# Kernel optimization log

Hardware: AMD Instinct MI355X
Metric: run time of the kernel (lower is better)

Reference implementation:

```python
import jax, jax.numpy as jnp
import numpy as np

N, B, S, F_DIM, E = 100000, 4096, 32, 256, 256


def _linear_params(key, fan_in, fan_out):
    kw, kb = jax.random.split(key)
    bound = 1.0 / np.sqrt(fan_in)
    W = jax.random.uniform(kw, (fan_in, fan_out), jnp.float32, -bound, bound)
    b = jax.random.uniform(kb, (fan_out,), jnp.float32, -bound, bound)
    return W, b


def setup_inputs() -> dict:
    key = jax.random.key(0)
    ks = jax.random.split(key, 10)
    Wm, bm = _linear_params(ks[4], F_DIM, E)
    Wq, bq = _linear_params(ks[5], F_DIM, E)
    Wk, bk = _linear_params(ks[6], F_DIM, E)
    Wv, bv = _linear_params(ks[7], F_DIM, E)
    Wc, bc = _linear_params(ks[8], 2 * E, E)
    return {
        "nodes": jax.random.randint(ks[0], (B,), 0, N),
        "neigh_mean": jax.random.randint(ks[1], (B, S), 0, N),
        "neigh_attn": jax.random.randint(ks[2], (B, S), 0, N),
        "id2feat": jax.random.normal(ks[3], (N, F_DIM), jnp.float32),
        "Wm": Wm, "bm": bm,
        "Wq": Wq, "bq": bq,
        "Wk": Wk, "bk": bk,
        "Wv": Wv, "bv": bv,
        "Wc": Wc, "bc": bc,
    }


def reference(nodes, neigh_mean, neigh_attn, id2feat,
              Wm, bm, Wq, bq, Wk, bk, Wv, bv, Wc, bc):
    self_feats = id2feat[nodes]                                   # [B, F]

    # MeanAggregator1: per-row mean of W(id2feat[neighbors]).
    # (mean(W x + b) == W mean(x) + b by linearity; all rows have S neighbors)
    ctx = jnp.mean(id2feat[neigh_mean], axis=1) @ Wm + bm          # [B, E]

    # AttnAggregator1: self-query attention over [neighbors ; self].
    neigh = id2feat[neigh_attn]                                    # [B, S, F]
    cat = jnp.concatenate([neigh, self_feats[:, None, :]], axis=1)  # [B, S+1, F]
    Q = self_feats @ Wq + bq                                       # [B, E]
    K = cat @ Wk + bk                                              # [B, S+1, E]
    V = cat @ Wv + bv                                              # [B, S+1, E]
    scores = jnp.einsum('be,bse->bs', Q, K)                        # [B, S+1]
    # Torch mask loop with uniform neighbor length S masks column S (the self slot)
    pad_mask = jnp.arange(S + 1) >= S                              # [S+1]
    scores = jnp.where(pad_mask[None, :], -jnp.inf, scores)
    attn = jax.nn.softmax(scores, axis=-1)
    mix = jnp.einsum('bs,bse->be', attn, V)                        # [B, E]

    combined = jnp.tanh(jnp.concatenate([mix, ctx], axis=-1) @ Wc + bc)  # [B, E]
    norm = jnp.linalg.norm(combined, axis=-1, keepdims=True)
    return combined / jnp.maximum(norm, 1e-12)                     # F.normalize(p=2)
```

## Files before the change

### kernel.cpp

```cpp
#include <hip/hip_runtime.h>
#include <hip/hip_fp16.h>
#include <math.h>

#define S_NEI 32

__global__ __launch_bounds__(256) void transpose256(const float* __restrict__ in,
                                                    float* __restrict__ outT) {
    __shared__ float tile[32][33];
    const int bx = blockIdx.x * 32, by = blockIdx.y * 32;
    const int x = threadIdx.x, y = threadIdx.y;
#pragma unroll
    for (int i = 0; i < 32; i += 8)
        tile[y + i][x] = in[(by + y + i) * 256 + bx + x];
    __syncthreads();
#pragma unroll
    for (int i = 0; i < 32; i += 8)
        outT[(bx + y + i) * 256 + by + x] = tile[x][y + i];
}

template <int KT>
__device__ __forceinline__ void gemm_tile8(const float* __restrict__ A, int row0,
                                           const float* __restrict__ B,
                                           float acc[2][4], float* __restrict__ sA,
                                           float* __restrict__ sB) {
    const int t = threadIdx.x;
    const int tr = t >> 6, tc = t & 63;
    const int r = t >> 5;
    const int k1 = t & 31;
    const size_t arow = (size_t)(row0 + r) * KT;
    for (int kb = 0; kb < KT; kb += 32) {
        sA[k1 * 12 + r] = A[arow + kb + k1];
#pragma unroll
        for (int i = 0; i < 8; ++i) {
            *reinterpret_cast<float4*>(&sB[(i * 4 + tr) * 256 + tc * 4]) =
                *reinterpret_cast<const float4*>(&B[(size_t)(kb + i * 4 + tr) * 256 + tc * 4]);
        }
        __syncthreads();
#pragma unroll
        for (int k = 0; k < 32; ++k) {
            const float2 a2 = *reinterpret_cast<const float2*>(&sA[k * 12 + tr * 2]);
            const float4 b4 = *reinterpret_cast<const float4*>(&sB[k * 256 + tc * 4]);
            acc[0][0] += a2.x * b4.x; acc[0][1] += a2.x * b4.y;
            acc[0][2] += a2.x * b4.z; acc[0][3] += a2.x * b4.w;
            acc[1][0] += a2.y * b4.x; acc[1][1] += a2.y * b4.y;
            acc[1][2] += a2.y * b4.z; acc[1][3] += a2.y * b4.w;
        }
        __syncthreads();
    }
}

__global__ __launch_bounds__(256) void precompute3(const float* __restrict__ Wq,
                                                   const float* __restrict__ Wv,
                                                   const float* __restrict__ Wm,
                                                   const float* __restrict__ Wc,
                                                   const float* __restrict__ WkT,
                                                   __half* __restrict__ Wqk,
                                                   __half* __restrict__ Wfused) {
    __shared__ float sA[32 * 12];
    __shared__ float sB[32 * 256];
    float acc[2][4] = {};
    const float *Ap, *Bp;
    __half* Cp;
    switch (blockIdx.y) {
        case 0: Ap = Wq; Bp = WkT; Cp = Wqk; break;
        case 1: Ap = Wv; Bp = Wc; Cp = Wfused; break;
        default: Ap = Wm; Bp = Wc + 256 * 256; Cp = Wfused + 256 * 256; break;
    }
    const int row0 = blockIdx.x * 8;
    gemm_tile8<256>(Ap, row0, Bp, acc, sA, sB);
    const int tr = threadIdx.x >> 6, tc = threadIdx.x & 63;
#pragma unroll
    for (int i = 0; i < 2; ++i) {
        const __half2 h0 = __floats2half2_rn(acc[i][0], acc[i][1]);
        const __half2 h1 = __floats2half2_rn(acc[i][2], acc[i][3]);
        __half2* dst = reinterpret_cast<__half2*>(&Cp[(size_t)(row0 + tr * 2 + i) * 256 + tc * 4]);
        dst[0] = h0;
        dst[1] = h1;
    }
}

__global__ __launch_bounds__(256) void bias_k(const float* __restrict__ bq,
                                              const float* __restrict__ bv,
                                              const float* __restrict__ bm,
                                              const float* __restrict__ bc,
                                              const float* __restrict__ Wc,
                                              const float* __restrict__ WkT,
                                              float* __restrict__ bqk,
                                              float* __restrict__ bfull) {
    const int c = blockIdx.x;
    const int e = threadIdx.x;
    const int w = e >> 6, l = e & 63;
    float a = bq[e] * WkT[e * 256 + c];
    float v = bv[e] * Wc[e * 256 + c] + bm[e] * Wc[(256 + e) * 256 + c];
    __shared__ float redA[4], redV[4];
#pragma unroll
    for (int off = 32; off; off >>= 1) { a += __shfl_xor(a, off); v += __shfl_xor(v, off); }
    if (l == 0) { redA[w] = a; redV[w] = v; }
    __syncthreads();
    if (e == 0) {
        bqk[c] = redA[0] + redA[1] + redA[2] + redA[3];
        bfull[c] = bc[c] + redV[0] + redV[1] + redV[2] + redV[3];
    }
}


#define SAF4(k) ((k) * 4 + ((((k) >> 3)) << 2))

#define FMA44(a4, b4)                                                       \
    do {                                                                    \
        acc[0][0] += (a4).x * (b4).x; acc[0][1] += (a4).x * (b4).y;         \
        acc[0][2] += (a4).x * (b4).z; acc[0][3] += (a4).x * (b4).w;         \
        acc[1][0] += (a4).y * (b4).x; acc[1][1] += (a4).y * (b4).y;         \
        acc[1][2] += (a4).y * (b4).z; acc[1][3] += (a4).y * (b4).w;         \
        acc[2][0] += (a4).z * (b4).x; acc[2][1] += (a4).z * (b4).y;         \
        acc[2][2] += (a4).z * (b4).z; acc[2][3] += (a4).z * (b4).w;         \
        acc[3][0] += (a4).w * (b4).x; acc[3][1] += (a4).w * (b4).y;         \
        acc[3][2] += (a4).w * (b4).z; acc[3][3] += (a4).w * (b4).w;         \
    } while (0)

__device__ __forceinline__ float4 h4_to_f4(float2 raw) {
    const __half2* h = reinterpret_cast<const __half2*>(&raw);
    const float2 f0 = __half22float2(h[0]);
    const float2 f1 = __half22float2(h[1]);
    return make_float4(f0.x, f0.y, f1.x, f1.y);
}

__global__ __launch_bounds__(256, 2) void fused4(const float* __restrict__ id2feat,
                                                 const int* __restrict__ nodes,
                                                 const int* __restrict__ neigh_mean,
                                                 const int* __restrict__ neigh_attn,
                                                 const __half* __restrict__ Wqk,
                                                 const float* __restrict__ bqk,
                                                 const __half* __restrict__ Wfused,
                                                 const float* __restrict__ bfull,
                                                 float* __restrict__ out) {
    __shared__ __align__(16) char smem[18112];
    float* R0  = (float*)smem;
    float* sQk = (float*)(smem + 12480);
    int*   sIA = (int*)(smem + 16640);
    int*   sIM = (int*)(smem + 17152);

    const int t = threadIdx.x;
    const int w = t >> 6, l = t & 63;
    const int kq = w;
    const int col4 = l * 4;
    const int row0 = blockIdx.x * 4;

    if (t < 128) sIA[t] = neigh_attn[(size_t)row0 * S_NEI + t];
    else sIM[t - 128] = neigh_mean[(size_t)row0 * S_NEI + (t - 128)];

    {
        const float4 v = *reinterpret_cast<const float4*>(
            &id2feat[(size_t)nodes[row0 + w] * 256 + col4]);
        R0[SAF4(col4 + 0) + w] = v.x;
        R0[SAF4(col4 + 1) + w] = v.y;
        R0[SAF4(col4 + 2) + w] = v.z;
        R0[SAF4(col4 + 3) + w] = v.w;
    }
    __syncthreads();

    float acc[4][4] = {};

    {
        const __half* Bp = Wqk + (size_t)(kq * 64) * 256 + col4;
        float2 bufA[8], bufB[8];
#pragma unroll
        for (int j = 0; j < 8; ++j)
            bufA[j] = *reinterpret_cast<const float2*>(&Bp[(size_t)j * 256]);
        for (int kb = 0; kb < 64; kb += 16) {
#pragma unroll
            for (int j = 0; j < 8; ++j)
                bufB[j] = *reinterpret_cast<const float2*>(&Bp[(size_t)(kb + 8 + j) * 256]);
#pragma unroll
            for (int j = 0; j < 8; ++j) {
                const float4 a4 = *reinterpret_cast<const float4*>(&R0[SAF4(kq * 64 + kb + j)]);
                const float4 b4 = h4_to_f4(bufA[j]);
                FMA44(a4, b4);
            }
            if (kb + 16 < 64) {
#pragma unroll
                for (int j = 0; j < 8; ++j)
                    bufA[j] = *reinterpret_cast<const float2*>(&Bp[(size_t)(kb + 16 + j) * 256]);
            }
#pragma unroll
            for (int j = 0; j < 8; ++j) {
                const float4 a4 =
                    *reinterpret_cast<const float4*>(&R0[SAF4(kq * 64 + kb + 8 + j)]);
                const float4 b4 = h4_to_f4(bufB[j]);
                FMA44(a4, b4);
            }
        }
    }
    __syncthreads();
    if (kq) {
        float* p = R0 + ((kq - 1) * 4) * 260 + col4;
#pragma unroll
        for (int r = 0; r < 4; ++r) {
            p[r * 260 + 0] = acc[r][0]; p[r * 260 + 1] = acc[r][1];
            p[r * 260 + 2] = acc[r][2]; p[r * 260 + 3] = acc[r][3];
        }
    }
    __syncthreads();
    if (kq == 0) {
        const float4 bq4 = *reinterpret_cast<const float4*>(&bqk[col4]);
#pragma unroll
        for (int r = 0; r < 4; ++r) {
            float v0 = acc[r][0] + bq4.x, v1 = acc[r][1] + bq4.y;
            float v2 = acc[r][2] + bq4.z, v3 = acc[r][3] + bq4.w;
#pragma unroll
            for (int s = 0; s < 3; ++s) {
                const float* p = R0 + (s * 4 + r) * 260 + col4;
                v0 += p[0]; v1 += p[1]; v2 += p[2]; v3 += p[3];
            }
            sQk[r * 260 + col4 + 0] = v0; sQk[r * 260 + col4 + 1] = v1;
            sQk[r * 260 + col4 + 2] = v2; sQk[r * 260 + col4 + 3] = v3;
        }
    }
    __syncthreads();

    {
        const int b = w;
        const float4 q = *reinterpret_cast<const float4*>(&sQk[b * 260 + col4]);
        const float4* f4 = reinterpret_cast<const float4*>(id2feat);
        const int* ia = sIA + b * 32;
        const int* im = sIM + b * 32;
        float4 macc = make_float4(0.f, 0.f, 0.f, 0.f);
        float4 wa = make_float4(0.f, 0.f, 0.f, 0.f);
        float m = -1e30f, e = 0.f;
#pragma unroll
        for (int cch = 0; cch < 4; ++cch) {
            float4 r[8];
#pragma unroll
            for (int j = 0; j < 8; ++j) r[j] = f4[(size_t)ia[cch * 8 + j] * 64 + l];
#pragma unroll
            for (int j = 0; j < 8; ++j) {
                const float4 v = f4[(size_t)im[cch * 8 + j] * 64 + l];
                macc.x += v.x; macc.y += v.y; macc.z += v.z; macc.w += v.w;
            }
            float p[8];
#pragma unroll
            for (int j = 0; j < 8; ++j) {
                float s = q.x * r[j].x + q.y * r[j].y + q.z * r[j].z + q.w * r[j].w;
#pragma unroll
                for (int off = 32; off; off >>= 1) s += __shfl_xor(s, off);
                p[j] = s;
            }
            float cm = p[0];
#pragma unroll
            for (int j = 1; j < 8; ++j) cm = fmaxf(cm, p[j]);
            const float newm = fmaxf(m, cm);
            const float sc = __expf(m - newm);
            e *= sc; wa.x *= sc; wa.y *= sc; wa.z *= sc; wa.w *= sc;
#pragma unroll
            for (int j = 0; j < 8; ++j) {
                const float g = __expf(p[j] - newm);
                e += g;
                wa.x += g * r[j].x; wa.y += g * r[j].y;
                wa.z += g * r[j].z; wa.w += g * r[j].w;
            }
            m = newm;
        }
        const float inv = 1.0f / e;
        const float mixv[4] = {wa.x * inv, wa.y * inv, wa.z * inv, wa.w * inv};
        const float mev[4] = {macc.x * (1.f / 32), macc.y * (1.f / 32),
                              macc.z * (1.f / 32), macc.w * (1.f / 32)};
#pragma unroll
        for (int c = 0; c < 4; ++c) {
            R0[SAF4(col4 + c) + b] = mixv[c];
            R0[SAF4(256 + col4 + c) + b] = mev[c];
        }
    }
    __syncthreads();

#pragma unroll
    for (int r = 0; r < 4; ++r)
#pragma unroll
        for (int c = 0; c < 4; ++c) acc[r][c] = 0.f;
    {
        const __half* Bp = Wfused + (size_t)(kq * 128) * 256 + col4;
        float2 bufA[8], bufB[8];
#pragma unroll
        for (int j = 0; j < 8; ++j)
            bufA[j] = *reinterpret_cast<const float2*>(&Bp[(size_t)j * 256]);
        for (int kb = 0; kb < 128; kb += 16) {
#pragma unroll
            for (int j = 0; j < 8; ++j)
                bufB[j] = *reinterpret_cast<const float2*>(&Bp[(size_t)(kb + 8 + j) * 256]);
#pragma unroll
            for (int j = 0; j < 8; ++j) {
                const float4 a4 =
                    *reinterpret_cast<const float4*>(&R0[SAF4(kq * 128 + kb + j)]);
                const float4 b4 = h4_to_f4(bufA[j]);
                FMA44(a4, b4);
            }
            if (kb + 16 < 128) {
#pragma unroll
                for (int j = 0; j < 8; ++j)
                    bufA[j] = *reinterpret_cast<const float2*>(&Bp[(size_t)(kb + 16 + j) * 256]);
            }
#pragma unroll
            for (int j = 0; j < 8; ++j) {
                const float4 a4 =
                    *reinterpret_cast<const float4*>(&R0[SAF4(kq * 128 + kb + 8 + j)]);
                const float4 b4 = h4_to_f4(bufB[j]);
                FMA44(a4, b4);
            }
        }
    }
    __syncthreads();
    if (kq) {
        float* p = R0 + ((kq - 1) * 4) * 260 + col4;
#pragma unroll
        for (int r = 0; r < 4; ++r) {
            p[r * 260 + 0] = acc[r][0]; p[r * 260 + 1] = acc[r][1];
            p[r * 260 + 2] = acc[r][2]; p[r * 260 + 3] = acc[r][3];
        }
    }
    __syncthreads();
    if (kq == 0) {
        const float4 bf4 = *reinterpret_cast<const float4*>(&bfull[col4]);
#pragma unroll
        for (int r = 0; r < 4; ++r) {
            float v0 = acc[r][0] + bf4.x, v1 = acc[r][1] + bf4.y;
            float v2 = acc[r][2] + bf4.z, v3 = acc[r][3] + bf4.w;
#pragma unroll
            for (int s = 0; s < 3; ++s) {
                const float* p = R0 + (s * 4 + r) * 260 + col4;
                v0 += p[0]; v1 += p[1]; v2 += p[2]; v3 += p[3];
            }
            v0 = tanhf(v0); v1 = tanhf(v1); v2 = tanhf(v2); v3 = tanhf(v3);
            float sq = v0 * v0 + v1 * v1 + v2 * v2 + v3 * v3;
#pragma unroll
            for (int off = 32; off; off >>= 1) sq += __shfl_xor(sq, off);
            const float invn = 1.0f / fmaxf(sqrtf(sq), 1e-12f);
            *reinterpret_cast<float4*>(&out[(size_t)(row0 + r) * 256 + col4]) =
                make_float4(v0 * invn, v1 * invn, v2 * invn, v3 * invn);
        }
    }
}

extern "C" void kernel_launch(void* const* d_in, const int* in_sizes, int n_in,
                              void* d_out, int out_size, void* d_ws, size_t ws_size,
                              hipStream_t stream) {
    const int* nodes      = (const int*)d_in[0];
    const int* neigh_mean = (const int*)d_in[1];
    const int* neigh_attn = (const int*)d_in[2];
    const float* id2feat  = (const float*)d_in[3];
    const float* Wm = (const float*)d_in[4];
    const float* bm = (const float*)d_in[5];
    const float* Wq = (const float*)d_in[6];
    const float* bq = (const float*)d_in[7];
    const float* Wk = (const float*)d_in[8];
    const float* Wv = (const float*)d_in[10];
    const float* bv = (const float*)d_in[11];
    const float* Wc = (const float*)d_in[12];
    const float* bc = (const float*)d_in[13];
    float* out = (float*)d_out;

    const int B = in_sizes[0];

    float* ws      = (float*)d_ws;
    float* WkT     = ws;
    __half* Wqk_h  = (__half*)(ws + 65536);
    __half* Wfus_h = (__half*)(ws + 98304);
    float* bqk     = ws + 163840;
    float* bfull   = ws + 164096;

    transpose256<<<dim3(8, 8), dim3(32, 8), 0, stream>>>(Wk, WkT);
    precompute3<<<dim3(32, 3), 256, 0, stream>>>(Wq, Wv, Wm, Wc, WkT, Wqk_h, Wfus_h);
    bias_k<<<256, 256, 0, stream>>>(bq, bv, bm, bc, Wc, WkT, bqk, bfull);
    fused4<<<B / 4, 256, 0, stream>>>(id2feat, nodes, neigh_mean, neigh_attn,
                                      Wqk_h, bqk, Wfus_h, bfull, out);
}
```

Measured before the change: 78.20 us.

## Process two rows per block and split neighbor gather across wave pairs

The fused kernel now handles 2 batch rows per block instead of 4, doubling the grid to B/2 blocks. Each row's 32-neighbor gather and online softmax is split across two waves (16 neighbors each), and the partial max, sum, weighted-V and mean results are merged through shared memory with a rescale. This raises parallelism and memory-level concurrency for the gather phase. In exchange, each block reads the fp16 weight matrices for only half as many rows, which doubles total weight traffic, and an extra sync and merge step is added.

```diff
diff --git a/kernel.cpp b/kernel.cpp
--- a/kernel.cpp
+++ b/kernel.cpp
@@ -104,18 +104,14 @@
 }
 
 
-#define SAF4(k) ((k) * 4 + ((((k) >> 3)) << 2))
-
-#define FMA44(a4, b4)                                                       \
+#define SAF2(k) ((k) * 2 + (((k) >> 3) << 1))
+
+#define FMA24(a2, b4)                                                       \
     do {                                                                    \
-        acc[0][0] += (a4).x * (b4).x; acc[0][1] += (a4).x * (b4).y;         \
-        acc[0][2] += (a4).x * (b4).z; acc[0][3] += (a4).x * (b4).w;         \
-        acc[1][0] += (a4).y * (b4).x; acc[1][1] += (a4).y * (b4).y;         \
-        acc[1][2] += (a4).y * (b4).z; acc[1][3] += (a4).y * (b4).w;         \
-        acc[2][0] += (a4).z * (b4).x; acc[2][1] += (a4).z * (b4).y;         \
-        acc[2][2] += (a4).z * (b4).z; acc[2][3] += (a4).z * (b4).w;         \
-        acc[3][0] += (a4).w * (b4).x; acc[3][1] += (a4).w * (b4).y;         \
-        acc[3][2] += (a4).w * (b4).z; acc[3][3] += (a4).w * (b4).w;         \
+        acc[0][0] += (a2).x * (b4).x; acc[0][1] += (a2).x * (b4).y;         \
+        acc[0][2] += (a2).x * (b4).z; acc[0][3] += (a2).x * (b4).w;         \
+        acc[1][0] += (a2).y * (b4).x; acc[1][1] += (a2).y * (b4).y;         \
+        acc[1][2] += (a2).y * (b4).z; acc[1][3] += (a2).y * (b4).w;         \
     } while (0)
 
 __device__ __forceinline__ float4 h4_to_f4(float2 raw) {
@@ -125,7 +121,7 @@
     return make_float4(f0.x, f0.y, f1.x, f1.y);
 }
 
-__global__ __launch_bounds__(256, 2) void fused4(const float* __restrict__ id2feat,
+__global__ __launch_bounds__(256, 2) void fused2(const float* __restrict__ id2feat,
                                                  const int* __restrict__ nodes,
                                                  const int* __restrict__ neigh_mean,
                                                  const int* __restrict__ neigh_attn,
@@ -134,32 +130,33 @@
                                                  const __half* __restrict__ Wfused,
                                                  const float* __restrict__ bfull,
                                                  float* __restrict__ out) {
-    __shared__ __align__(16) char smem[18112];
-    float* R0  = (float*)smem;
-    float* sQk = (float*)(smem + 12480);
-    int*   sIA = (int*)(smem + 16640);
-    int*   sIM = (int*)(smem + 17152);
+    __shared__ __align__(16) char smem[15456];
+    float* RA  = (float*)smem;
+    float* RB  = (float*)(smem + 4608);
+    float* sQk = (float*)(smem + 12864);
+    int*   sIA = (int*)(smem + 14944);
+    int*   sIM = (int*)(smem + 15200);
 
     const int t = threadIdx.x;
     const int w = t >> 6, l = t & 63;
     const int kq = w;
     const int col4 = l * 4;
-    const int row0 = blockIdx.x * 4;
-
-    if (t < 128) sIA[t] = neigh_attn[(size_t)row0 * S_NEI + t];
-    else sIM[t - 128] = neigh_mean[(size_t)row0 * S_NEI + (t - 128)];
-
-    {
+    const int row0 = blockIdx.x * 2;
+
+    if (t < 64) sIA[t] = neigh_attn[(size_t)row0 * S_NEI + t];
+    else if (t < 128) sIM[t - 64] = neigh_mean[(size_t)row0 * S_NEI + (t - 64)];
+
+    if (w < 2) {
         const float4 v = *reinterpret_cast<const float4*>(
             &id2feat[(size_t)nodes[row0 + w] * 256 + col4]);
-        R0[SAF4(col4 + 0) + w] = v.x;
-        R0[SAF4(col4 + 1) + w] = v.y;
-        R0[SAF4(col4 + 2) + w] = v.z;
-        R0[SAF4(col4 + 3) + w] = v.w;
-    }
-    __syncthreads();
-
-    float acc[4][4] = {};
+        RA[SAF2(col4 + 0) + w] = v.x;
+        RA[SAF2(col4 + 1) + w] = v.y;
+        RA[SAF2(col4 + 2) + w] = v.z;
+        RA[SAF2(col4 + 3) + w] = v.w;
+    }
+    __syncthreads();
+
+    float acc[2][4] = {};
 
     {
         const __half* Bp = Wqk + (size_t)(kq * 64) * 256 + col4;
@@ -173,9 +170,9 @@
                 bufB[j] = *reinterpret_cast<const float2*>(&Bp[(size_t)(kb + 8 + j) * 256]);
 #pragma unroll
             for (int j = 0; j < 8; ++j) {
-                const float4 a4 = *reinterpret_cast<const float4*>(&R0[SAF4(kq * 64 + kb + j)]);
+                const float2 a2 = *reinterpret_cast<const float2*>(&RA[SAF2(kq * 64 + kb + j)]);
                 const float4 b4 = h4_to_f4(bufA[j]);
-                FMA44(a4, b4);
+                FMA24(a2, b4);
             }
             if (kb + 16 < 64) {
 #pragma unroll
@@ -184,18 +181,18 @@
             }
 #pragma unroll
             for (int j = 0; j < 8; ++j) {
-                const float4 a4 =
-                    *reinterpret_cast<const float4*>(&R0[SAF4(kq * 64 + kb + 8 + j)]);
+                const float2 a2 =
+                    *reinterpret_cast<const float2*>(&RA[SAF2(kq * 64 + kb + 8 + j)]);
                 const float4 b4 = h4_to_f4(bufB[j]);
-                FMA44(a4, b4);
+                FMA24(a2, b4);
             }
         }
     }
     __syncthreads();
     if (kq) {
-        float* p = R0 + ((kq - 1) * 4) * 260 + col4;
-#pragma unroll
-        for (int r = 0; r < 4; ++r) {
+        float* p = RB + ((kq - 1) * 2) * 260 + col4;
+#pragma unroll
+        for (int r = 0; r < 2; ++r) {
             p[r * 260 + 0] = acc[r][0]; p[r * 260 + 1] = acc[r][1];
             p[r * 260 + 2] = acc[r][2]; p[r * 260 + 3] = acc[r][3];
         }
@@ -204,12 +201,12 @@
     if (kq == 0) {
         const float4 bq4 = *reinterpret_cast<const float4*>(&bqk[col4]);
 #pragma unroll
-        for (int r = 0; r < 4; ++r) {
+        for (int r = 0; r < 2; ++r) {
             float v0 = acc[r][0] + bq4.x, v1 = acc[r][1] + bq4.y;
             float v2 = acc[r][2] + bq4.z, v3 = acc[r][3] + bq4.w;
 #pragma unroll
             for (int s = 0; s < 3; ++s) {
-                const float* p = R0 + (s * 4 + r) * 260 + col4;
+                const float* p = RB + (s * 2 + r) * 260 + col4;
                 v0 += p[0]; v1 += p[1]; v2 += p[2]; v3 += p[3];
             }
             sQk[r * 260 + col4 + 0] = v0; sQk[r * 260 + col4 + 1] = v1;
@@ -218,17 +215,17 @@
     }
     __syncthreads();
 
+    float4 wa = make_float4(0.f, 0.f, 0.f, 0.f);
+    float4 macc = make_float4(0.f, 0.f, 0.f, 0.f);
+    float m = -1e30f, e = 0.f;
     {
-        const int b = w;
+        const int b = w >> 1, h = w & 1;
         const float4 q = *reinterpret_cast<const float4*>(&sQk[b * 260 + col4]);
         const float4* f4 = reinterpret_cast<const float4*>(id2feat);
-        const int* ia = sIA + b * 32;
-        const int* im = sIM + b * 32;
-        float4 macc = make_float4(0.f, 0.f, 0.f, 0.f);
-        float4 wa = make_float4(0.f, 0.f, 0.f, 0.f);
-        float m = -1e30f, e = 0.f;
-#pragma unroll
-        for (int cch = 0; cch < 4; ++cch) {
+        const int* ia = sIA + b * 32 + h * 16;
+        const int* im = sIM + b * 32 + h * 16;
+#pragma unroll
+        for (int cch = 0; cch < 2; ++cch) {
             float4 r[8];
 #pragma unroll
             for (int j = 0; j < 8; ++j) r[j] = f4[(size_t)ia[cch * 8 + j] * 64 + l];
@@ -260,20 +257,42 @@
             }
             m = newm;
         }
-        const float inv = 1.0f / e;
-        const float mixv[4] = {wa.x * inv, wa.y * inv, wa.z * inv, wa.w * inv};
-        const float mev[4] = {macc.x * (1.f / 32), macc.y * (1.f / 32),
-                              macc.z * (1.f / 32), macc.w * (1.f / 32)};
+    }
+    {
+        float4* sW = (float4*)RB;
+        float4* sM = (float4*)(RB + 1024);
+        float* sME = RB + 2048;
+        sW[w * 64 + l] = wa;
+        sM[w * 64 + l] = macc;
+        if (l == 0) { sME[w * 2] = m; sME[w * 2 + 1] = e; }
+    }
+    __syncthreads();
+    if ((w & 1) == 0) {
+        const int b = w >> 1;
+        const float4* sW = (const float4*)RB;
+        const float4* sM = (const float4*)(RB + 1024);
+        const float* sME = RB + 2048;
+        const float m0 = sME[w * 2], e0 = sME[w * 2 + 1];
+        const float m1 = sME[(w + 1) * 2], e1 = sME[(w + 1) * 2 + 1];
+        const float M = fmaxf(m0, m1);
+        const float f0 = __expf(m0 - M), f1 = __expf(m1 - M);
+        const float inv = 1.0f / (e0 * f0 + e1 * f1);
+        const float4 w0 = sW[w * 64 + l], w1 = sW[(w + 1) * 64 + l];
+        const float4 c0 = sM[w * 64 + l], c1 = sM[(w + 1) * 64 + l];
+        const float mixv[4] = {(w0.x * f0 + w1.x * f1) * inv, (w0.y * f0 + w1.y * f1) * inv,
+                               (w0.z * f0 + w1.z * f1) * inv, (w0.w * f0 + w1.w * f1) * inv};
+        const float mev[4] = {(c0.x + c1.x) * (1.f / 32), (c0.y + c1.y) * (1.f / 32),
+                              (c0.z + c1.z) * (1.f / 32), (c0.w + c1.w) * (1.f / 32)};
 #pragma unroll
         for (int c = 0; c < 4; ++c) {
-            R0[SAF4(col4 + c) + b] = mixv[c];
-            R0[SAF4(256 + col4 + c) + b] = mev[c];
-        }
-    }
-    __syncthreads();
-
-#pragma unroll
-    for (int r = 0; r < 4; ++r)
+            RA[SAF2(col4 + c) + b] = mixv[c];
+            RA[SAF2(256 + col4 + c) + b] = mev[c];
+        }
+    }
+    __syncthreads();
+
+#pragma unroll
+    for (int r = 0; r < 2; ++r)
 #pragma unroll
         for (int c = 0; c < 4; ++c) acc[r][c] = 0.f;
     {
@@ -288,10 +307,10 @@
                 bufB[j] = *reinterpret_cast<const float2*>(&Bp[(size_t)(kb + 8 + j) * 256]);
 #pragma unroll
             for (int j = 0; j < 8; ++j) {
-                const float4 a4 =
-                    *reinterpret_cast<const float4*>(&R0[SAF4(kq * 128 + kb + j)]);
+                const float2 a2 =
+                    *reinterpret_cast<const float2*>(&RA[SAF2(kq * 128 + kb + j)]);
                 const float4 b4 = h4_to_f4(bufA[j]);
-                FMA44(a4, b4);
+                FMA24(a2, b4);
             }
             if (kb + 16 < 128) {
 #pragma unroll
@@ -300,18 +319,18 @@
             }
 #pragma unroll
             for (int j = 0; j < 8; ++j) {
-                const float4 a4 =
-                    *reinterpret_cast<const float4*>(&R0[SAF4(kq * 128 + kb + 8 + j)]);
+                const float2 a2 =
+                    *reinterpret_cast<const float2*>(&RA[SAF2(kq * 128 + kb + 8 + j)]);
                 const float4 b4 = h4_to_f4(bufB[j]);
-                FMA44(a4, b4);
+                FMA24(a2, b4);
             }
         }
     }
     __syncthreads();
     if (kq) {
-        float* p = R0 + ((kq - 1) * 4) * 260 + col4;
-#pragma unroll
-        for (int r = 0; r < 4; ++r) {
+        float* p = RB + ((kq - 1) * 2) * 260 + col4;
+#pragma unroll
+        for (int r = 0; r < 2; ++r) {
             p[r * 260 + 0] = acc[r][0]; p[r * 260 + 1] = acc[r][1];
             p[r * 260 + 2] = acc[r][2]; p[r * 260 + 3] = acc[r][3];
         }
@@ -320,12 +339,12 @@
     if (kq == 0) {
         const float4 bf4 = *reinterpret_cast<const float4*>(&bfull[col4]);
 #pragma unroll
-        for (int r = 0; r < 4; ++r) {
+        for (int r = 0; r < 2; ++r) {
             float v0 = acc[r][0] + bf4.x, v1 = acc[r][1] + bf4.y;
             float v2 = acc[r][2] + bf4.z, v3 = acc[r][3] + bf4.w;
 #pragma unroll
             for (int s = 0; s < 3; ++s) {
-                const float* p = R0 + (s * 4 + r) * 260 + col4;
+                const float* p = RB + (s * 2 + r) * 260 + col4;
                 v0 += p[0]; v1 += p[1]; v2 += p[2]; v3 += p[3];
             }
             v0 = tanhf(v0); v1 = tanhf(v1); v2 = tanhf(v2); v3 = tanhf(v3);
@@ -369,6 +388,6 @@
     transpose256<<<dim3(8, 8), dim3(32, 8), 0, stream>>>(Wk, WkT);
     precompute3<<<dim3(32, 3), 256, 0, stream>>>(Wq, Wv, Wm, Wc, WkT, Wqk_h, Wfus_h);
     bias_k<<<256, 256, 0, stream>>>(bq, bv, bm, bc, Wc, WkT, bqk, bfull);
-    fused4<<<B / 4, 256, 0, stream>>>(id2feat, nodes, neigh_mean, neigh_attn,
+    fused2<<<B / 2, 256, 0, stream>>>(id2feat, nodes, neigh_mean, neigh_attn,
                                       Wqk_h, bqk, Wfus_h, bfull, out);
 }
```

Result: slower. 89.29 us (+14.2%).
